# Kernel tuning notes

Measured on AMD Instinct MI355X. Metric: run time of the kernel, lower is better.

The kernel has to match this reference:

```python
import jax, jax.numpy as jnp
import numpy as np

NUM_CLASSES = 10
EPS = 1e-8  # torch F.cosine_similarity norm clamp


def setup_inputs() -> dict:
    key = jax.random.key(0)
    k1, k2, k3 = jax.random.split(key, 3)
    pred = jax.random.normal(k1, (4096, 128), dtype=jnp.float32)
    target = jax.random.randint(k2, (4096,), 0, NUM_CLASSES, dtype=jnp.int64)
    W = jax.random.normal(k3, (NUM_CLASSES, 128), dtype=jnp.float32)  # cos() class weights
    return {"pred": pred, "target": target, "W": W}


def reference(pred, target, W):
    N, D = pred.shape
    C = NUM_CLASSES
    f32 = pred.dtype

    # pairwise difference norms via GEMM identity (avoids NxNxD tensor)
    sq = jnp.sum(pred * pred, axis=-1)                       # [N]
    G = pred @ pred.T                                        # [N,N]
    d2 = jnp.maximum(sq[:, None] + sq[None, :] - 2.0 * G, 0.0)
    dn = jnp.maximum(jnp.sqrt(d2 + 1e-16), EPS)              # ||f_a - f_b|| clamped

    proj = pred @ W.T                                        # [N,C] = w_i . f
    wn = jnp.maximum(jnp.sqrt(jnp.sum(W * W, axis=-1)), EPS) # [C]

    counts = jnp.zeros((C,), dtype=jnp.int32).at[target].add(1)  # N per class
    exist = jnp.sum(counts > 0).astype(f32)
    Nt = counts[target].astype(f32)                          # N[target[b]] per sample

    loss1 = jnp.zeros((), f32)
    loss2 = jnp.zeros((), f32)
    for i in range(C):
        pos = target == i
        # pair (a in class i, b not in class i); sum order-invariant vs original
        mask = pos[:, None] & (~pos)[None, :]
        Ni = jnp.maximum(counts[i], 1).astype(f32)
        w_pair = jnp.where(mask, 1.0 / (Nt[None, :] * Ni), 0.0)  # 1/(N_j*N_i)
        pi = proj[:, i]
        # cosine_similarity(f_a - f_b, w_i)
        M = (pi[:, None] - pi[None, :]) / (wn[i] * dn)
        l1 = jnp.sum(w_pair * (1.0 - M) ** 2) / (exist - 1.0)
        # detached-margin statistics (same values in forward)
        mm = jnp.sum(w_pair * M) / (exist - 1.0)
        mv = jnp.sum(w_pair * (M - mm) ** 2) / (exist - 1.0)
        valid = counts[i] > 0
        loss1 = loss1 + jnp.where(valid, l1, 0.0)
        loss2 = loss2 + jnp.where(valid, jnp.abs(mv / mm), 0.0)

    loss1 = loss1 / exist
    loss2 = loss2 / exist
    return (loss1, loss2)
```

## Files before the change

kernel.cpp:

```cpp
#include <hip/hip_runtime.h>

#define WS_SACC   0
#define WS_DONE   128
#define WS_GCUR   192
#define WS_INVWN  896
#define WS_PERM   1024
#define WS_SQBF   165888
#define WS_PROJ   182272
#define WS_PREDBF 346112

#define NCLS 10
#define NROW 4096
#define DDIM 128
#define MAXT 42
#define GRID_MAIN (MAXT * MAXT)

typedef __attribute__((ext_vector_type(8))) short short8;
typedef __attribute__((ext_vector_type(4))) float f32x4;

#define AS3(p) ((__attribute__((address_space(3))) void*)(p))
#define AS1(p) ((const __attribute__((address_space(1))) void*)(p))

__device__ __forceinline__ unsigned short f2bf(float x) {
  unsigned int u = __float_as_uint(x);
  u += 0x7FFFu + ((u >> 16) & 1u);
  return (unsigned short)(u >> 16);
}
__device__ __forceinline__ float bf2f(unsigned short b) {
  return __uint_as_float(((unsigned int)b) << 16);
}

__global__ void __launch_bounds__(256)
k_rows(const float* __restrict__ pred, const float* __restrict__ W,
       const int* __restrict__ tgt, char* __restrict__ ws) {
  __shared__ float Wl[NCLS * DDIM];
  __shared__ int lcnt[NCLS];
  __shared__ int gbase_s[NCLS];
  int t = threadIdx.x;
  if (t < NCLS) lcnt[t] = 0;
  for (int s = t; s < NCLS * DDIM; s += 256) Wl[s] = W[s];
  __syncthreads();

  if (t < 160) {
    int c = t >> 4, ln = t & 15;
    float sw = 0.f;
#pragma unroll
    for (int k = 0; k < 8; k++) { float w = Wl[c * DDIM + ln * 8 + k]; sw = fmaf(w, w, sw); }
    sw += __shfl_xor(sw, 1, 64);
    sw += __shfl_xor(sw, 2, 64);
    sw += __shfl_xor(sw, 4, 64);
    sw += __shfl_xor(sw, 8, 64);
    if (ln == 0) ((float*)(ws + WS_INVWN))[c] = 1.0f / fmaxf(sqrtf(sw), 1e-8f);
  }

  int row  = blockIdx.x * 32 + (t >> 3);
  int part = t & 7;
  const float4* p4 = (const float4*)(pred + row * DDIM + part * 16);
  unsigned short* pb = ((unsigned short*)(ws + WS_PREDBF)) + row * DDIM + part * 16;

  float4 v[4];
  float ss = 0.f;
#pragma unroll
  for (int ch = 0; ch < 4; ch++) {
    v[ch] = p4[ch];
    unsigned short b0 = f2bf(v[ch].x), b1 = f2bf(v[ch].y),
                   b2 = f2bf(v[ch].z), b3 = f2bf(v[ch].w);
    float r0 = bf2f(b0), r1 = bf2f(b1), r2 = bf2f(b2), r3 = bf2f(b3);
    ss = fmaf(r0, r0, ss); ss = fmaf(r1, r1, ss);
    ss = fmaf(r2, r2, ss); ss = fmaf(r3, r3, ss);
    ushort4 u; u.x = b0; u.y = b1; u.z = b2; u.w = b3;
    *((ushort4*)(pb + ch * 4)) = u;
  }
  float acc[NCLS];
#pragma unroll
  for (int c = 0; c < NCLS; c++) acc[c] = 0.f;
#pragma unroll
  for (int c = 0; c < NCLS; c++) {
#pragma unroll
    for (int ch = 0; ch < 4; ch++) {
      float4 w = *(const float4*)&Wl[c * DDIM + part * 16 + ch * 4];
      acc[c] = fmaf(v[ch].x, w.x, acc[c]);
      acc[c] = fmaf(v[ch].y, w.y, acc[c]);
      acc[c] = fmaf(v[ch].z, w.z, acc[c]);
      acc[c] = fmaf(v[ch].w, w.w, acc[c]);
    }
  }
#pragma unroll
  for (int m = 1; m <= 4; m <<= 1) {
    ss += __shfl_xor(ss, m, 64);
#pragma unroll
    for (int c = 0; c < NCLS; c++) acc[c] += __shfl_xor(acc[c], m, 64);
  }
  int myc = 0, lslot = 0;
  if (part == 0) {
    ((float*)(ws + WS_SQBF))[row] = ss;
    float* proj = (float*)(ws + WS_PROJ);
#pragma unroll
    for (int c = 0; c < NCLS; c++) proj[row * NCLS + c] = acc[c];
    myc = tgt[row];
    lslot = atomicAdd(&lcnt[myc], 1);
  }
  __syncthreads();
  if (t < NCLS) {
    int n = lcnt[t];
    gbase_s[t] = (n > 0) ? atomicAdd((int*)(ws + WS_GCUR + t * 64), n) : 0;
  }
  __syncthreads();
  if (part == 0) {
    ((int*)(ws + WS_PERM))[myc * NROW + gbase_s[myc] + lslot] = row;
  }
}

__global__ void __launch_bounds__(256)
k_main(char* __restrict__ ws, float* __restrict__ out) {
  const int t = threadIdx.x;
  int h[NCLS];
#pragma unroll
  for (int c = 0; c < NCLS; c++) h[c] = *((const int*)(ws + WS_GCUR + c * 64));

  int at = blockIdx.x / MAXT, bt = blockIdx.x % MAXT;
  int acc = 0, clsA = 0, ka = 0, clsB = 0, kb = 0;
#pragma unroll
  for (int c = 0; c < NCLS; c++) {
    int tc = (h[c] + 127) >> 7;
    if (at >= acc && at < acc + tc) { clsA = c; ka = at - acc; }
    if (bt >= acc && bt < acc + tc) { clsB = c; kb = bt - acc; }
    acc += tc;
  }
  const int ntiles = acc;
  const bool active = (at < ntiles) && (bt < ntiles) && (clsA != clsB);

  int bias = 0;
  if (active) {
    const int avcnt = min(128, h[clsA] - ka * 128);
    const int bvcnt = min(128, h[clsB] - kb * 128);
    const float wg = (1.0f / (float)h[clsA]) * (1.0f / (float)h[clsB]);
    const float invwn_cls = ((const float*)(ws + WS_INVWN))[clsA];

    __shared__ __align__(16) char Btile[128 * 256];
    __shared__ __align__(16) float sqa_s[128], pa_s[128];
    __shared__ float sqb_s[128], pnb_s[128];
    __shared__ int   brow_s[128], arow_s[128];
    __shared__ float red_s[4][2];

    const float* sqbf = (const float*)(ws + WS_SQBF);
    const float* proj = (const float*)(ws + WS_PROJ);
    const int*   perm = (const int*)(ws + WS_PERM);
    const unsigned short* predbf = (const unsigned short*)(ws + WS_PREDBF);

    if (t < 128) {
      bool valid = t < bvcnt;
      int brow = valid ? perm[clsB * NROW + kb * 128 + t] : 0;
      brow_s[t] = brow;
      sqb_s[t] = valid ? sqbf[brow] + 1e-16f : __builtin_inff();
      pnb_s[t] = valid ? proj[brow * NCLS + clsA] * invwn_cls : 0.0f;
    } else {
      int i = t - 128;
      bool valid = i < avcnt;
      int arow = valid ? perm[clsA * NROW + ka * 128 + i] : 0;
      arow_s[i] = arow;
      sqa_s[i] = valid ? sqbf[arow] : __builtin_inff();
      pa_s[i]  = proj[arow * NCLS + clsA] * invwn_cls;
    }
    __syncthreads();

#pragma unroll
    for (int it = 0; it < 8; it++) {
      int s = it * 256 + t;
      int r = s >> 4, cc = (s & 15) ^ (r & 15);
      const unsigned short* gp = predbf + brow_s[r] * DDIM + cc * 8;
      __builtin_amdgcn_global_load_lds(AS1(gp), AS3(Btile + s * 16), 16, 0, 0);
    }

    const int lane = t & 63, w = t >> 6;
    const int l16 = lane & 15, quad = lane >> 4;

    short8 afrag[2][4];
    f32x4 sqa4[2], pa4[2];
#pragma unroll
    for (int fi = 0; fi < 2; fi++) {
      const unsigned short* ap = predbf + arow_s[w * 32 + fi * 16 + l16] * DDIM + quad * 8;
#pragma unroll
      for (int kk = 0; kk < 4; kk++) afrag[fi][kk] = *(const short8*)(ap + kk * 32);
      int m0 = w * 32 + fi * 16 + quad * 4;
      sqa4[fi] = *(const f32x4*)(sqa_s + m0);
      pa4[fi]  = *(const f32x4*)(pa_s + m0);
    }
    __syncthreads();

    float S1 = 0.f, S2 = 0.f;
#pragma unroll
    for (int s = 0; s < 8; s++) {
      int rb = s * 16 + l16;
      short8 bfrag[4];
#pragma unroll
      for (int kk = 0; kk < 4; kk++)
        bfrag[kk] = *(const short8*)(Btile + rb * 256 + (((quad + kk * 4) ^ l16) * 16));
      float sqb = sqb_s[rb], pnb = pnb_s[rb];
#pragma unroll
      for (int fi = 0; fi < 2; fi++) {
        f32x4 g = {0.f, 0.f, 0.f, 0.f};
#pragma unroll
        for (int kk = 0; kk < 4; kk++)
          g = __builtin_amdgcn_mfma_f32_16x16x32_bf16(afrag[fi][kk], bfrag[kk], g, 0, 0, 0);
#pragma unroll
        for (int r = 0; r < 4; r++) {
          float d2 = fmaf(-2.0f, g[r], sqa4[fi][r] + sqb);
          float rin = rsqrtf(d2);
          float M = (pa4[fi][r] - pnb) * rin;
          S1 += M;
          S2 = fmaf(M, M, S2);
        }
      }
    }

#pragma unroll
    for (int off = 32; off > 0; off >>= 1) {
      S1 += __shfl_xor(S1, off, 64);
      S2 += __shfl_xor(S2, off, 64);
    }
    if (lane == 0) { red_s[w][0] = S1; red_s[w][1] = S2; }
    __syncthreads();
    if (t == 0) {
      float a1 = (red_s[0][0] + red_s[1][0]) + (red_s[2][0] + red_s[3][0]);
      float a2 = (red_s[0][1] + red_s[1][1]) + (red_s[2][1] + red_s[3][1]);
      float* Sacc = (float*)(ws + WS_SACC);
      float o1 = __hip_atomic_fetch_add(&Sacc[clsA], wg * a1,
                                        __ATOMIC_RELAXED, __HIP_MEMORY_SCOPE_AGENT);
      float o2 = __hip_atomic_fetch_add(&Sacc[10 + clsA], wg * a2,
                                        __ATOMIC_RELAXED, __HIP_MEMORY_SCOPE_AGENT);
      bias = (o1 == -1e30f && o2 == -1e30f) ? 1 : 0;
    }
  }

  if (t == 0) {
    int old = __hip_atomic_fetch_add((int*)(ws + WS_DONE), 1 + bias,
                                     __ATOMIC_RELAXED, __HIP_MEMORY_SCOPE_AGENT);
    if (old == GRID_MAIN - 1) {
      float* Sacc = (float*)(ws + WS_SACC);
      float exist = 0.f;
      for (int c = 0; c < NCLS; c++) if (h[c] > 0) exist += 1.f;
      float em1 = exist - 1.0f;
      float l1 = 0.f, l2 = 0.f;
      for (int c = 0; c < NCLS; c++) {
        if (h[c] <= 0) continue;
        float s1 = __hip_atomic_load(&Sacc[c],      __ATOMIC_RELAXED, __HIP_MEMORY_SCOPE_AGENT);
        float s2 = __hip_atomic_load(&Sacc[10 + c], __ATOMIC_RELAXED, __HIP_MEMORY_SCOPE_AGENT);
        l1 += (em1 - 2.f * s1 + s2) / em1;
        float mm = s1 / em1;
        float mv = s2 / em1 - mm * mm;
        l2 += fabsf(mv / mm);
      }
      out[0] = l1 / exist;
      out[1] = l2 / exist;
    }
  }
}

extern "C" void kernel_launch(void* const* d_in, const int* in_sizes, int n_in,
                              void* d_out, int out_size, void* d_ws, size_t ws_size,
                              hipStream_t stream) {
  const float* pred = (const float*)d_in[0];
  const int*   tgt  = (const int*)d_in[1];
  const float* W    = (const float*)d_in[2];
  float* out = (float*)d_out;
  char*  ws  = (char*)d_ws;

  hipMemsetAsync(ws, 0, 1024, stream);
  k_rows<<<NROW / 32, 256, 0, stream>>>(pred, W, tgt, ws);
  k_main<<<GRID_MAIN, 256, 0, stream>>>(ws, out);
}
```

Before: 112.7 us.

## Replace atomic last-block reduction with per-block partials and final kernel

Drops the global float atomics and the done-counter last-block pattern in the main kernel. Each block now writes its two partial sums to a workspace slot, and a new single-block kernel reduces them per class and computes the losses. The row kernel also moves to 16 rows per block so more blocks run, and it builds the class permutation before the projection work. The cost is a third kernel launch and an extra pass over the partials array.

```diff
diff --git a/kernel.cpp b/kernel.cpp
--- a/kernel.cpp
+++ b/kernel.cpp
@@ -1,13 +1,12 @@
 #include <hip/hip_runtime.h>
 
-#define WS_SACC   0
-#define WS_DONE   128
 #define WS_GCUR   192
 #define WS_INVWN  896
-#define WS_PERM   1024
-#define WS_SQBF   165888
-#define WS_PROJ   182272
-#define WS_PREDBF 346112
+#define WS_PART   2048
+#define WS_SQBF   16384
+#define WS_PROJ   32768
+#define WS_PERM   196608
+#define WS_PREDBF 360448
 
 #define NCLS 10
 #define NROW 4096
@@ -36,13 +35,27 @@
   __shared__ float Wl[NCLS * DDIM];
   __shared__ int lcnt[NCLS];
   __shared__ int gbase_s[NCLS];
+  __shared__ int lslot_s[16];
+  __shared__ int cls_s[16];
   int t = threadIdx.x;
   if (t < NCLS) lcnt[t] = 0;
   for (int s = t; s < NCLS * DDIM; s += 256) Wl[s] = W[s];
   __syncthreads();
 
-  if (t < 160) {
-    int c = t >> 4, ln = t & 15;
+  if (t < 16) {
+    int myrow = blockIdx.x * 16 + t;
+    int c = tgt[myrow];
+    cls_s[t] = c;
+    lslot_s[t] = atomicAdd(&lcnt[c], 1);
+  }
+  __syncthreads();
+  if (t < NCLS) {
+    int n = lcnt[t];
+    gbase_s[t] = (n > 0) ? atomicAdd((int*)(ws + WS_GCUR + t * 64), n) : 0;
+  }
+  if (t >= 64 && t < 224) {
+    int i = t - 64;
+    int c = i >> 4, ln = i & 15;
     float sw = 0.f;
 #pragma unroll
     for (int k = 0; k < 8; k++) { float w = Wl[c * DDIM + ln * 8 + k]; sw = fmaf(w, w, sw); }
@@ -52,16 +65,21 @@
     sw += __shfl_xor(sw, 8, 64);
     if (ln == 0) ((float*)(ws + WS_INVWN))[c] = 1.0f / fmaxf(sqrtf(sw), 1e-8f);
   }
-
-  int row  = blockIdx.x * 32 + (t >> 3);
-  int part = t & 7;
-  const float4* p4 = (const float4*)(pred + row * DDIM + part * 16);
-  unsigned short* pb = ((unsigned short*)(ws + WS_PREDBF)) + row * DDIM + part * 16;
-
-  float4 v[4];
+  __syncthreads();
+  if (t < 16) {
+    int c = cls_s[t];
+    ((int*)(ws + WS_PERM))[c * NROW + gbase_s[c] + lslot_s[t]] = blockIdx.x * 16 + t;
+  }
+
+  int row  = blockIdx.x * 16 + (t >> 4);
+  int part = t & 15;
+  const float4* p4 = (const float4*)(pred + row * DDIM + part * 8);
+  unsigned short* pb = ((unsigned short*)(ws + WS_PREDBF)) + row * DDIM + part * 8;
+
+  float4 v[2];
   float ss = 0.f;
 #pragma unroll
-  for (int ch = 0; ch < 4; ch++) {
+  for (int ch = 0; ch < 2; ch++) {
     v[ch] = p4[ch];
     unsigned short b0 = f2bf(v[ch].x), b1 = f2bf(v[ch].y),
                    b2 = f2bf(v[ch].z), b3 = f2bf(v[ch].w);
@@ -77,8 +95,8 @@
 #pragma unroll
   for (int c = 0; c < NCLS; c++) {
 #pragma unroll
-    for (int ch = 0; ch < 4; ch++) {
-      float4 w = *(const float4*)&Wl[c * DDIM + part * 16 + ch * 4];
+    for (int ch = 0; ch < 2; ch++) {
+      float4 w = *(const float4*)&Wl[c * DDIM + part * 8 + ch * 4];
       acc[c] = fmaf(v[ch].x, w.x, acc[c]);
       acc[c] = fmaf(v[ch].y, w.y, acc[c]);
       acc[c] = fmaf(v[ch].z, w.z, acc[c]);
@@ -86,33 +104,21 @@
     }
   }
 #pragma unroll
-  for (int m = 1; m <= 4; m <<= 1) {
+  for (int m = 1; m <= 8; m <<= 1) {
     ss += __shfl_xor(ss, m, 64);
 #pragma unroll
     for (int c = 0; c < NCLS; c++) acc[c] += __shfl_xor(acc[c], m, 64);
   }
-  int myc = 0, lslot = 0;
   if (part == 0) {
     ((float*)(ws + WS_SQBF))[row] = ss;
     float* proj = (float*)(ws + WS_PROJ);
 #pragma unroll
     for (int c = 0; c < NCLS; c++) proj[row * NCLS + c] = acc[c];
-    myc = tgt[row];
-    lslot = atomicAdd(&lcnt[myc], 1);
-  }
-  __syncthreads();
-  if (t < NCLS) {
-    int n = lcnt[t];
-    gbase_s[t] = (n > 0) ? atomicAdd((int*)(ws + WS_GCUR + t * 64), n) : 0;
-  }
-  __syncthreads();
-  if (part == 0) {
-    ((int*)(ws + WS_PERM))[myc * NROW + gbase_s[myc] + lslot] = row;
   }
 }
 
 __global__ void __launch_bounds__(256)
-k_main(char* __restrict__ ws, float* __restrict__ out) {
+k_main(char* __restrict__ ws) {
   const int t = threadIdx.x;
   int h[NCLS];
 #pragma unroll
@@ -130,7 +136,7 @@
   const int ntiles = acc;
   const bool active = (at < ntiles) && (bt < ntiles) && (clsA != clsB);
 
-  int bias = 0;
+  float p1 = 0.f, p2 = 0.f;
   if (active) {
     const int avcnt = min(128, h[clsA] - ka * 128);
     const int bvcnt = min(128, h[clsB] - kb * 128);
@@ -222,38 +228,62 @@
     if (lane == 0) { red_s[w][0] = S1; red_s[w][1] = S2; }
     __syncthreads();
     if (t == 0) {
-      float a1 = (red_s[0][0] + red_s[1][0]) + (red_s[2][0] + red_s[3][0]);
-      float a2 = (red_s[0][1] + red_s[1][1]) + (red_s[2][1] + red_s[3][1]);
-      float* Sacc = (float*)(ws + WS_SACC);
-      float o1 = __hip_atomic_fetch_add(&Sacc[clsA], wg * a1,
-                                        __ATOMIC_RELAXED, __HIP_MEMORY_SCOPE_AGENT);
-      float o2 = __hip_atomic_fetch_add(&Sacc[10 + clsA], wg * a2,
-                                        __ATOMIC_RELAXED, __HIP_MEMORY_SCOPE_AGENT);
-      bias = (o1 == -1e30f && o2 == -1e30f) ? 1 : 0;
+      p1 = wg * ((red_s[0][0] + red_s[1][0]) + (red_s[2][0] + red_s[3][0]));
+      p2 = wg * ((red_s[0][1] + red_s[1][1]) + (red_s[2][1] + red_s[3][1]));
     }
   }
 
   if (t == 0) {
-    int old = __hip_atomic_fetch_add((int*)(ws + WS_DONE), 1 + bias,
-                                     __ATOMIC_RELAXED, __HIP_MEMORY_SCOPE_AGENT);
-    if (old == GRID_MAIN - 1) {
-      float* Sacc = (float*)(ws + WS_SACC);
-      float exist = 0.f;
-      for (int c = 0; c < NCLS; c++) if (h[c] > 0) exist += 1.f;
-      float em1 = exist - 1.0f;
-      float l1 = 0.f, l2 = 0.f;
-      for (int c = 0; c < NCLS; c++) {
-        if (h[c] <= 0) continue;
-        float s1 = __hip_atomic_load(&Sacc[c],      __ATOMIC_RELAXED, __HIP_MEMORY_SCOPE_AGENT);
-        float s2 = __hip_atomic_load(&Sacc[10 + c], __ATOMIC_RELAXED, __HIP_MEMORY_SCOPE_AGENT);
-        l1 += (em1 - 2.f * s1 + s2) / em1;
-        float mm = s1 / em1;
-        float mv = s2 / em1 - mm * mm;
-        l2 += fabsf(mv / mm);
-      }
-      out[0] = l1 / exist;
-      out[1] = l2 / exist;
-    }
+    float* part = (float*)(ws + WS_PART);
+    part[blockIdx.x * 2]     = p1;
+    part[blockIdx.x * 2 + 1] = p2;
+  }
+}
+
+__global__ void __launch_bounds__(256)
+k_final(char* __restrict__ ws, float* __restrict__ out) {
+  __shared__ float Sred[2 * NCLS];
+  __shared__ int tcls_s[MAXT];
+  int t = threadIdx.x;
+  if (t < 2 * NCLS) Sred[t] = 0.f;
+  __shared__ int h_s[NCLS];
+  if (t < NCLS) h_s[t] = *((const int*)(ws + WS_GCUR + t * 64));
+  __syncthreads();
+  if (t == 0) {
+    int nb = 0;
+    for (int c = 0; c < NCLS; c++) {
+      int tc = (h_s[c] + 127) >> 7;
+      for (int i = 0; i < tc && nb + i < MAXT; i++) tcls_s[nb + i] = c;
+      nb += tc;
+    }
+    for (int i = nb; i < MAXT; i++) tcls_s[i] = 0;
+  }
+  __syncthreads();
+  const float* part = (const float*)(ws + WS_PART);
+  for (int i = t; i < GRID_MAIN; i += 256) {
+    int c = tcls_s[i / MAXT];
+    float v1 = part[i * 2], v2 = part[i * 2 + 1];
+    if (v1 != 0.f || v2 != 0.f) {
+      atomicAdd(&Sred[c], v1);
+      atomicAdd(&Sred[NCLS + c], v2);
+    }
+  }
+  __syncthreads();
+  if (t == 0) {
+    float exist = 0.f;
+    for (int c = 0; c < NCLS; c++) if (h_s[c] > 0) exist += 1.f;
+    float em1 = exist - 1.0f;
+    float l1 = 0.f, l2 = 0.f;
+    for (int c = 0; c < NCLS; c++) {
+      if (h_s[c] <= 0) continue;
+      float s1 = Sred[c], s2 = Sred[NCLS + c];
+      l1 += (em1 - 2.f * s1 + s2) / em1;
+      float mm = s1 / em1;
+      float mv = s2 / em1 - mm * mm;
+      l2 += fabsf(mv / mm);
+    }
+    out[0] = l1 / exist;
+    out[1] = l2 / exist;
   }
 }
 
@@ -267,6 +297,7 @@
   char*  ws  = (char*)d_ws;
 
   hipMemsetAsync(ws, 0, 1024, stream);
-  k_rows<<<NROW / 32, 256, 0, stream>>>(pred, W, tgt, ws);
-  k_main<<<GRID_MAIN, 256, 0, stream>>>(ws, out);
-}
+  k_rows<<<NROW / 16, 256, 0, stream>>>(pred, W, tgt, ws);
+  k_main<<<GRID_MAIN, 256, 0, stream>>>(ws);
+  k_final<<<1, 256, 0, stream>>>(ws, out);
+}
```

After: 93.05 us. -17.4%, faster.
